# Kernel tuning notes

Measured on AMD Instinct MI355X. Metric: run time of the kernel, lower is better.

The kernel has to match this reference:

```python
import jax, jax.numpy as jnp
import numpy as np
from jax import lax

J = 8  # number of wavelet levels


def _dwconv1d(x, w, dilation):
    # x: (B, ch, T+pad), w: (ch, 1, L) depthwise (grouped, groups=ch) conv,
    # cross-correlation semantics matching torch.nn.functional.conv1d.
    ch = x.shape[1]
    return lax.conv_general_dilated(
        x, w, window_strides=(1,), padding='VALID',
        rhs_dilation=(dilation,),
        dimension_numbers=('NCH', 'OIH', 'NCH'),
        feature_group_count=ch)


def _fwd_j1(x, h0, h1):
    # Level-1 UDT-CWT: pad, roll, channel-concat, depthwise conv per filter.
    b, ch, T = x.shape

    def branch(h):
        L = h.shape[-1]
        p = L - 1
        xp = jnp.pad(x, ((0, 0), (0, 0), (p // 2, p - p // 2)))
        xp = jnp.concatenate([xp, jnp.roll(xp, -1, axis=-1)], axis=1)  # (B, 2ch, T+p)
        w = jnp.tile(h, (2 * ch, 1, 1))  # (2ch, 1, L)
        return _dwconv1d(xp, w, 1)  # (B, 2ch, T)

    return branch(h0), branch(h1)


def _fwd_j2plus(x, h0a, h1a, h0b, h1b, dilation):
    # Level 2+ UDT-CWT: alternating a/b tree filters, dilated depthwise conv.
    b, ch, T = x.shape

    def branch(ha, hb):
        h = jnp.concatenate([ha, hb], axis=0)        # (2, 1, L)
        w = jnp.tile(h, (ch // 2, 1, 1))              # (ch, 1, L) -> a,b,a,b,...
        L = h.shape[-1]
        p = (L - 1) * dilation
        xp = jnp.pad(x, ((0, 0), (0, 0), (p // 2, p - p // 2)))
        return _dwconv1d(xp, w, dilation)             # (B, ch, T)

    return branch(h0a, h0b), branch(h1a, h1b)


def _udtcwt(x, h0o, h1o, h0a, h1a, h0b, h1b):
    B, C, T = x.shape
    if T % 2 != 0:
        x = jnp.concatenate([x, x[:, :, -1:]], axis=-1)
    x_phi, x_psi = _fwd_j1(x, h0o, h1o)
    # swap channel halves of the high-pass output
    x_psi = jnp.concatenate([x_psi[:, C:2 * C, :], x_psi[:, :C, :]], axis=1)
    x_psis = [x_psi]
    for j in range(1, J):
        if x_phi.shape[-1] % 4 != 0:
            x_phi = jnp.concatenate(
                [x_phi[:, :, 0:1], x_phi, x_phi[:, :, -1:]], axis=-1)
        x_phi, x_psi = _fwd_j2plus(x_phi, h0a, h1a, h0b, h1b, 2 ** j)
        x_psis.append(x_psi)
    yl = x_phi[:, :C, :]              # (B, C, T)
    yh = jnp.stack(x_psis, axis=0)    # (J, B, 2C, T) -- uniform since T % 4 == 0
    return yl, yh


def setup_inputs() -> dict:
    key = jax.random.key(0)
    ks = jax.random.split(key, 7)
    B, C, T = 4, 8, 65536
    return {
        'x':   jax.random.normal(ks[0], (B, C, T), dtype=jnp.float32),
        'h0o': jax.random.normal(ks[1], (1, 1, 5), dtype=jnp.float32) * 0.3,
        'h1o': jax.random.normal(ks[2], (1, 1, 7), dtype=jnp.float32) * 0.3,
        'h0a': jax.random.normal(ks[3], (1, 1, 10), dtype=jnp.float32) * 0.3,
        'h1a': jax.random.normal(ks[4], (1, 1, 10), dtype=jnp.float32) * 0.3,
        'h0b': jax.random.normal(ks[5], (1, 1, 10), dtype=jnp.float32) * 0.3,
        'h1b': jax.random.normal(ks[6], (1, 1, 10), dtype=jnp.float32) * 0.3,
    }


def reference(x, h0o, h1o, h0a, h1a, h0b, h1b):
    return _udtcwt(x, h0o, h1o, h0a, h1a, h0b, h1b)
```

## Files before the change

kernel.cpp:

```cpp
#include <hip/hip_runtime.h>


static constexpr int B  = 4;
static constexpr int C2 = 16;
static constexpr int T  = 65536;

__device__ __forceinline__ float rfl(float x) {
    return __int_as_float(__builtin_amdgcn_readfirstlane(__float_as_int(x)));
}

__device__ __forceinline__ int PH(int p) { return p + (p >> 5); }

__device__ __forceinline__ void bar_lds() {
    asm volatile("s_waitcnt lgkmcnt(0)" ::: "memory");
    __builtin_amdgcn_s_barrier();
}

__device__ float g_phi4[(size_t)B * C2 * T];

static constexpr int NT1 = 256;
static constexpr int TS1 = 2048;
static constexpr int HB1 = 68;
static constexpr int S1  = TS1 + 2 * HB1;
static constexpr int SP1 = S1 + S1 / 32;

template <int SH>
__device__ __forceinline__ void k1_lvl1(
    const float* __restrict__ in, float* __restrict__ out,
    const float* __restrict__ h0o, const float* __restrict__ h1o,
    float* __restrict__ psi_g, int gbase, int tid)
{
    float f0[5], f1[7];
#pragma unroll
    for (int k = 0; k < 5; ++k) f0[k] = rfl(h0o[k]);
#pragma unroll
    for (int k = 0; k < 7; ++k) f1[k] = rfl(h1o[k]);

    constexpr int WO    = SH ? -3 : -2;
    constexpr int FS    = SH ? 2 : 0;
    constexpr int MO    = 64;
    constexpr int START = HB1 - MO;
    constexpr int END   = HB1 + TS1 + MO;

    for (int p4 = START + tid * 4; p4 < END; p4 += NT1 * 4) {
        float w[10];
#pragma unroll
        for (int k = 0; k < 10; ++k) w[k] = in[PH(p4 + WO + k)];
        float a[4];
#pragma unroll
        for (int i = 0; i < 4; ++i) {
            float s = 0.f;
#pragma unroll
            for (int k = 0; k < 5; ++k) s += w[i + k + FS] * f0[k];
            a[i] = s;
        }
        if ((unsigned)(p4 - HB1) < (unsigned)TS1) {
            float bb[4];
#pragma unroll
            for (int i = 0; i < 4; ++i) {
                float s = 0.f;
#pragma unroll
                for (int k = 0; k < 7; ++k) s += w[i + k] * f1[k];
                bb[i] = s;
            }
            *(float4*)&psi_g[gbase + p4] = make_float4(bb[0], bb[1], bb[2], bb[3]);
        }
        const bool inT = (unsigned)(gbase + p4) < (unsigned)T;
#pragma unroll
        for (int i = 0; i < 4; ++i) out[PH(p4 + i)] = inT ? a[i] : 0.f;
    }
}

template <int D, int W, int MO>
__device__ __forceinline__ void k1_level(
    float* __restrict__ in, float* __restrict__ out,
    const float (&f0)[10], const float (&f1)[10],
    int gbase, int tid)
{
    constexpr int HALF  = 9 * D / 2;
    constexpr int START = HB1 - MO;
    constexpr int N     = TS1 + 2 * MO;
    static_assert(N % D == 0, "");
    constexpr int NPD   = N / D;
    constexpr int CPC   = (NPD + W - 1) / W;
    constexpr int G     = D * CPC;
    static_assert(G <= NT1, "single chunk per thread required");
    constexpr int LOG2D = (D == 2 ? 1 : D == 4 ? 2 : 3);

    float a[W], bb[W];
    int p0 = 0;
    const bool act = tid < G;
    if (act) {
        int r  = tid & (D - 1);
        int q  = tid >> LOG2D;
        int ms = q * W;
        if (ms > NPD - W) ms = NPD - W;
        p0 = START + r + ms * D;

        float v[W + 9];
#pragma unroll
        for (int n = 0; n < W + 9; ++n) v[n] = in[PH(p0 - HALF + n * D)];
#pragma unroll
        for (int m = 0; m < W; ++m) { a[m] = 0.f; bb[m] = 0.f; }
#pragma unroll
        for (int k = 0; k < 10; ++k)
#pragma unroll
            for (int m = 0; m < W; ++m) {
                float x = v[m + k];
                a[m] += x * f0[k]; bb[m] += x * f1[k];
            }
    }
    bar_lds();
    if (act) {
#pragma unroll
        for (int m = 0; m < W; ++m) {
            int p = p0 + m * D;
            out[PH(p)] = ((unsigned)(gbase + p) < (unsigned)T) ? a[m] : 0.f;
            in[PH(p)]  = bb[m];
        }
    }
    bar_lds();
}

__device__ __forceinline__ void k1_copyout(
    const float* __restrict__ buf, float* __restrict__ dst, int tid)
{
    for (int i4 = tid * 4; i4 < TS1; i4 += NT1 * 4) {
        int ph = PH(HB1 + i4);
        *(float4*)&dst[i4] = make_float4(buf[ph], buf[ph+1], buf[ph+2], buf[ph+3]);
    }
}

__global__ __launch_bounds__(256, 6) void udtcwt_k1(
    const float* __restrict__ x,
    const float* __restrict__ h0o, const float* __restrict__ h1o,
    const float* __restrict__ h0a, const float* __restrict__ h1a,
    const float* __restrict__ h0b, const float* __restrict__ h1b,
    float* __restrict__ out)
{
    __shared__ float A[SP1];
    __shared__ float Bf[SP1];

    const int tid   = threadIdx.x;
    const int bid   = blockIdx.x;
    const int tile  = bid & 31;
    const int chain = bid >> 5;
    const int shbit = chain & 1;
    const int cx    = (chain >> 1) & 7;
    const int b     = chain >> 4;
    const int c2    = shbit * 8 + cx;
    const int t0    = tile * TS1;
    const int gbase = t0 - HB1;

    const float* xin = x + (size_t)(b * 8 + cx) * T;
    for (int i4 = tid * 4; i4 < S1; i4 += NT1 * 4) {
        int gg = gbase + i4;
        float4 v = ((unsigned)gg < (unsigned)T)
                 ? *(const float4*)&xin[gg]
                 : make_float4(0.f, 0.f, 0.f, 0.f);
        int ph = PH(i4);
        A[ph] = v.x; A[ph+1] = v.y; A[ph+2] = v.z; A[ph+3] = v.w;
    }

    float f0[10], f1[10];
    {
        const float* F0 = (c2 & 1) ? h0b : h0a;
        const float* F1 = (c2 & 1) ? h1b : h1a;
#pragma unroll
        for (int k = 0; k < 10; ++k) { f0[k] = rfl(F0[k]); f1[k] = rfl(F1[k]); }
    }

    float* yh   = out + (size_t)B * 8 * T;
    const size_t LS = (size_t)B * C2 * T;
    float* psi0 = yh + (size_t)(b * C2 + c2) * T;

    bar_lds();
    if (shbit) k1_lvl1<1>(A, Bf, h0o, h1o, psi0, gbase, tid);
    else       k1_lvl1<0>(A, Bf, h0o, h1o, psi0, gbase, tid);
    bar_lds();

    k1_level<2, 9, 54>(Bf, A, f0, f1, gbase, tid);
    k1_copyout(Bf, psi0 + 1 * LS + t0, tid);
    k1_level<4, 9, 36>(A, Bf, f0, f1, gbase, tid);
    k1_copyout(A, psi0 + 2 * LS + t0, tid);
    k1_level<8, 9, 0>(Bf, A, f0, f1, gbase, tid);
    k1_copyout(Bf, psi0 + 3 * LS + t0, tid);
    k1_copyout(A, g_phi4 + (size_t)(b * C2 + c2) * T + t0, tid);
}

static constexpr int NT2 = 768;
static constexpr int TS2 = 8192;
static constexpr int HB2 = 1080;
static constexpr int S2  = TS2 + 2 * HB2;

template <int D, int W, int MO, bool LAST>
__device__ __forceinline__ void k2_level(
    float* __restrict__ buf,
    const float (&f0)[10], const float (&f1)[10],
    float* __restrict__ psi_g, float* __restrict__ yl_g,
    int gbase, int tid, bool wr_yl)
{
    constexpr int HALF  = 9 * D / 2;
    constexpr int START = HB2 - MO;
    constexpr int N     = TS2 + 2 * MO;
    static_assert(N % D == 0, "");
    constexpr int NPD   = N / D;
    constexpr int CPC   = (NPD + W - 1) / W;
    constexpr int G     = D * CPC;
    static_assert(G <= NT2, "single chunk per thread required");
    constexpr int LOG2D = (D == 16 ? 4 : D == 32 ? 5 : D == 64 ? 6 : 7);

    float a[W], bb[W];
    int p0 = 0;
    const bool act = tid < G;
    const bool do_phi = !LAST || wr_yl;
    if (act) {
        int r  = tid & (D - 1);
        int q  = tid >> LOG2D;
        int ms = q * W;
        if (ms > NPD - W) ms = NPD - W;
        p0 = START + r + ms * D;

        float v[W + 9];
#pragma unroll
        for (int n = 0; n < W + 9; ++n) v[n] = buf[p0 - HALF + n * D];
#pragma unroll
        for (int m = 0; m < W; ++m) { a[m] = 0.f; bb[m] = 0.f; }
        if (do_phi) {
#pragma unroll
            for (int k = 0; k < 10; ++k)
#pragma unroll
                for (int m = 0; m < W; ++m) {
                    float x = v[m + k];
                    a[m] += x * f0[k]; bb[m] += x * f1[k];
                }
        } else {
#pragma unroll
            for (int k = 0; k < 10; ++k)
#pragma unroll
                for (int m = 0; m < W; ++m) bb[m] += v[m + k] * f1[k];
        }
    }
    bar_lds();
    if (act) {
#pragma unroll
        for (int m = 0; m < W; ++m) {
            int p = p0 + m * D;
            const bool core = (unsigned)(p - HB2) < (unsigned)TS2;
            if (core) psi_g[gbase + p] = bb[m];
            if constexpr (!LAST) {
                buf[p] = ((unsigned)(gbase + p) < (unsigned)T) ? a[m] : 0.f;
            } else {
                if (wr_yl && core) yl_g[gbase + p] = a[m];
            }
        }
    }
    bar_lds();
}

__global__ __launch_bounds__(768, 6) void udtcwt_k2(
    const float* __restrict__ h0a, const float* __restrict__ h1a,
    const float* __restrict__ h0b, const float* __restrict__ h1b,
    float* __restrict__ out)
{
    __shared__ float A[S2];

    const int tid   = threadIdx.x;
    const int bid   = blockIdx.x;
    const int tile  = bid & 7;
    const int chain = bid >> 3;
    const int shbit = chain & 1;
    const int cx    = (chain >> 1) & 7;
    const int b     = chain >> 4;
    const int c2    = shbit * 8 + cx;
    const int gbase = tile * TS2 - HB2;

    const float* pin = g_phi4 + (size_t)(b * C2 + c2) * T;
    for (int i4 = tid * 4; i4 < S2; i4 += NT2 * 4) {
        int gg = gbase + i4;
        float4 v = ((unsigned)gg < (unsigned)T)
                 ? *(const float4*)&pin[gg]
                 : make_float4(0.f, 0.f, 0.f, 0.f);
        *(float4*)&A[i4] = v;
    }

    float f0[10], f1[10];
    {
        const float* F0 = (c2 & 1) ? h0b : h0a;
        const float* F1 = (c2 & 1) ? h1b : h1a;
#pragma unroll
        for (int k = 0; k < 10; ++k) { f0[k] = rfl(F0[k]); f1[k] = rfl(F1[k]); }
    }

    float* yl_g = out + (size_t)(b * 8 + c2) * T;
    float* yh   = out + (size_t)B * 8 * T;
    const size_t LS = (size_t)B * C2 * T;
    float* psi0 = yh + (size_t)(b * C2 + c2) * T;
    const bool wr_yl = (c2 < 8);

    bar_lds();
    k2_level< 16, 15, 1008, false>(A, f0, f1, psi0 + 4 * LS, nullptr, gbase, tid, false);
    k2_level< 32, 15,  864, false>(A, f0, f1, psi0 + 5 * LS, nullptr, gbase, tid, false);
    k2_level< 64, 15,  576, false>(A, f0, f1, psi0 + 6 * LS, nullptr, gbase, tid, false);
    k2_level<128, 15,    0, true >(A, f0, f1, psi0 + 7 * LS, yl_g,    gbase, tid, wr_yl);
}

extern "C" void kernel_launch(void* const* d_in, const int* in_sizes, int n_in,
                              void* d_out, int out_size, void* d_ws, size_t ws_size,
                              hipStream_t stream)
{
    const float* x   = (const float*)d_in[0];
    const float* h0o = (const float*)d_in[1];
    const float* h1o = (const float*)d_in[2];
    const float* h0a = (const float*)d_in[3];
    const float* h1a = (const float*)d_in[4];
    const float* h0b = (const float*)d_in[5];
    const float* h1b = (const float*)d_in[6];

    udtcwt_k1<<<64 * (T / TS1), NT1, 0, stream>>>(x, h0o, h1o, h0a, h1a, h0b, h1b,
                                                  (float*)d_out);
    udtcwt_k2<<<64 * (T / TS2), NT2, 0, stream>>>(h0a, h1a, h0b, h1b,
                                                  (float*)d_out);
}
```

Before: 48.98 us.

## Double the level-1..4 tile size and drop LDS padding for vectorized LDS access

Doubles the first kernel's time tile from 2048 to 4096 samples and widens per-thread work (W 9→17), so each block recomputes proportionally less halo. It also removes the padded LDS indexing, which allows float4 LDS reads and writes in level 1, the staging load and the copy-out. Launch bounds drop from 6 to 4 waves to fit the larger LDS and register use. In exchange, strided dilated reads (D=2,4,8) may now hit bank conflicts without padding, and occupancy is lower.

```diff
diff --git a/kernel.cpp b/kernel.cpp
--- a/kernel.cpp
+++ b/kernel.cpp
@@ -9,8 +9,6 @@
     return __int_as_float(__builtin_amdgcn_readfirstlane(__float_as_int(x)));
 }
 
-__device__ __forceinline__ int PH(int p) { return p + (p >> 5); }
-
 __device__ __forceinline__ void bar_lds() {
     asm volatile("s_waitcnt lgkmcnt(0)" ::: "memory");
     __builtin_amdgcn_s_barrier();
@@ -19,10 +17,9 @@
 __device__ float g_phi4[(size_t)B * C2 * T];
 
 static constexpr int NT1 = 256;
-static constexpr int TS1 = 2048;
+static constexpr int TS1 = 4096;
 static constexpr int HB1 = 68;
 static constexpr int S1  = TS1 + 2 * HB1;
-static constexpr int SP1 = S1 + S1 / 32;
 
 template <int SH>
 __device__ __forceinline__ void k1_lvl1(
@@ -36,22 +33,28 @@
 #pragma unroll
     for (int k = 0; k < 7; ++k) f1[k] = rfl(h1o[k]);
 
-    constexpr int WO    = SH ? -3 : -2;
+    constexpr int OFF   = SH ? 1 : 2;
     constexpr int FS    = SH ? 2 : 0;
     constexpr int MO    = 64;
     constexpr int START = HB1 - MO;
     constexpr int END   = HB1 + TS1 + MO;
 
     for (int p4 = START + tid * 4; p4 < END; p4 += NT1 * 4) {
-        float w[10];
-#pragma unroll
-        for (int k = 0; k < 10; ++k) w[k] = in[PH(p4 + WO + k)];
+        float w[12];
+        {
+            float4 w0 = *(const float4*)&in[p4 - 4];
+            float4 w1 = *(const float4*)&in[p4];
+            float4 w2 = *(const float4*)&in[p4 + 4];
+            w[0]=w0.x; w[1]=w0.y; w[2]=w0.z; w[3]=w0.w;
+            w[4]=w1.x; w[5]=w1.y; w[6]=w1.z; w[7]=w1.w;
+            w[8]=w2.x; w[9]=w2.y; w[10]=w2.z; w[11]=w2.w;
+        }
         float a[4];
 #pragma unroll
         for (int i = 0; i < 4; ++i) {
             float s = 0.f;
 #pragma unroll
-            for (int k = 0; k < 5; ++k) s += w[i + k + FS] * f0[k];
+            for (int k = 0; k < 5; ++k) s += w[i + k + FS + OFF] * f0[k];
             a[i] = s;
         }
         if ((unsigned)(p4 - HB1) < (unsigned)TS1) {
@@ -60,14 +63,14 @@
             for (int i = 0; i < 4; ++i) {
                 float s = 0.f;
 #pragma unroll
-                for (int k = 0; k < 7; ++k) s += w[i + k] * f1[k];
+                for (int k = 0; k < 7; ++k) s += w[i + k + OFF] * f1[k];
                 bb[i] = s;
             }
             *(float4*)&psi_g[gbase + p4] = make_float4(bb[0], bb[1], bb[2], bb[3]);
         }
         const bool inT = (unsigned)(gbase + p4) < (unsigned)T;
-#pragma unroll
-        for (int i = 0; i < 4; ++i) out[PH(p4 + i)] = inT ? a[i] : 0.f;
+        *(float4*)&out[p4] = inT ? make_float4(a[0], a[1], a[2], a[3])
+                                 : make_float4(0.f, 0.f, 0.f, 0.f);
     }
 }
 
@@ -99,7 +102,7 @@
 
         float v[W + 9];
 #pragma unroll
-        for (int n = 0; n < W + 9; ++n) v[n] = in[PH(p0 - HALF + n * D)];
+        for (int n = 0; n < W + 9; ++n) v[n] = in[p0 - HALF + n * D];
 #pragma unroll
         for (int m = 0; m < W; ++m) { a[m] = 0.f; bb[m] = 0.f; }
 #pragma unroll
@@ -115,8 +118,8 @@
 #pragma unroll
         for (int m = 0; m < W; ++m) {
             int p = p0 + m * D;
-            out[PH(p)] = ((unsigned)(gbase + p) < (unsigned)T) ? a[m] : 0.f;
-            in[PH(p)]  = bb[m];
+            out[p] = ((unsigned)(gbase + p) < (unsigned)T) ? a[m] : 0.f;
+            in[p]  = bb[m];
         }
     }
     bar_lds();
@@ -126,25 +129,24 @@
     const float* __restrict__ buf, float* __restrict__ dst, int tid)
 {
     for (int i4 = tid * 4; i4 < TS1; i4 += NT1 * 4) {
-        int ph = PH(HB1 + i4);
-        *(float4*)&dst[i4] = make_float4(buf[ph], buf[ph+1], buf[ph+2], buf[ph+3]);
-    }
-}
-
-__global__ __launch_bounds__(256, 6) void udtcwt_k1(
+        *(float4*)&dst[i4] = *(const float4*)&buf[HB1 + i4];
+    }
+}
+
+__global__ __launch_bounds__(256, 4) void udtcwt_k1(
     const float* __restrict__ x,
     const float* __restrict__ h0o, const float* __restrict__ h1o,
     const float* __restrict__ h0a, const float* __restrict__ h1a,
     const float* __restrict__ h0b, const float* __restrict__ h1b,
     float* __restrict__ out)
 {
-    __shared__ float A[SP1];
-    __shared__ float Bf[SP1];
+    __shared__ float A[S1];
+    __shared__ float Bf[S1];
 
     const int tid   = threadIdx.x;
     const int bid   = blockIdx.x;
-    const int tile  = bid & 31;
-    const int chain = bid >> 5;
+    const int tile  = bid & 15;
+    const int chain = bid >> 4;
     const int shbit = chain & 1;
     const int cx    = (chain >> 1) & 7;
     const int b     = chain >> 4;
@@ -158,8 +160,7 @@
         float4 v = ((unsigned)gg < (unsigned)T)
                  ? *(const float4*)&xin[gg]
                  : make_float4(0.f, 0.f, 0.f, 0.f);
-        int ph = PH(i4);
-        A[ph] = v.x; A[ph+1] = v.y; A[ph+2] = v.z; A[ph+3] = v.w;
+        *(float4*)&A[i4] = v;
     }
 
     float f0[10], f1[10];
@@ -179,11 +180,11 @@
     else       k1_lvl1<0>(A, Bf, h0o, h1o, psi0, gbase, tid);
     bar_lds();
 
-    k1_level<2, 9, 54>(Bf, A, f0, f1, gbase, tid);
+    k1_level<2, 17, 54>(Bf, A, f0, f1, gbase, tid);
     k1_copyout(Bf, psi0 + 1 * LS + t0, tid);
-    k1_level<4, 9, 36>(A, Bf, f0, f1, gbase, tid);
+    k1_level<4, 17, 36>(A, Bf, f0, f1, gbase, tid);
     k1_copyout(A, psi0 + 2 * LS + t0, tid);
-    k1_level<8, 9, 0>(Bf, A, f0, f1, gbase, tid);
+    k1_level<8, 17, 0>(Bf, A, f0, f1, gbase, tid);
     k1_copyout(Bf, psi0 + 3 * LS + t0, tid);
     k1_copyout(A, g_phi4 + (size_t)(b * C2 + c2) * T + t0, tid);
 }
```

Result: faster. 47.15 us (-3.7%).
